# Kernel tuning notes

Hardware: AMD Instinct MI355X
Metric: run time of the kernel (lower is better)

Reference implementation:

```python
import jax, jax.numpy as jnp
import numpy as np

B, L, C = 4, 4096, 1024
H = 16
D = C // H  # head_dim = 64


def setup_inputs() -> dict:
    key = jax.random.key(0)
    k1, k2, k3 = jax.random.split(key, 3)
    x = jax.random.normal(k1, (B, L, C), dtype=jnp.float32)
    W_qkv = jax.random.normal(k2, (C, 3 * C), dtype=jnp.float32) * (C ** -0.5)
    W_proj = jax.random.normal(k3, (C, C), dtype=jnp.float32) * (C ** -0.5)
    b_proj = jnp.zeros((C,), dtype=jnp.float32)
    return {"x": x, "W_qkv": W_qkv, "W_proj": W_proj, "b_proj": b_proj}


def reference(x, W_qkv, W_proj, b_proj):
    Bx, Lx, Cx = x.shape
    # qkv projection (no bias), split into q,k,v each [B, H, L, D]
    qkv = (x @ W_qkv).reshape(Bx, Lx, 3, H, D).transpose(2, 0, 3, 1, 4)
    q, k, v = qkv[0], qkv[1], qkv[2]
    # elu+1 feature map
    q = jax.nn.elu(q) + 1.0
    k = jax.nn.elu(k) + 1.0
    # Faithful to source einsums: kv[b,h,d,m] = sum_n k[b,h,n,d] v[b,h,n,m]
    kv = jnp.einsum('bhnd,bhnm->bhdm', k, v)
    # out[b,h,l,d] = sum_n q[b,h,l,n] * sum_m kv[b,h,d,m] (as written in source)
    out = jnp.einsum('bhln,bhdm->bhld', q, kv)
    out = out.transpose(0, 2, 1, 3).reshape(Bx, Lx, Cx)
    # output projection with bias; dropouts are identity (p=0)
    return out @ W_proj + b_proj
```

## Files before the change

### kernel.cpp

```cpp
#include <hip/hip_runtime.h>
#include <stdint.h>

#define BB 4
#define LL 4096
#define CC 1024
#define HH 16
#define DD 64
#define MTOT (BB*LL)
#define NQK 2048

typedef __attribute__((ext_vector_type(4))) float f32x4;
typedef __attribute__((ext_vector_type(8))) short bf16x8;
typedef __attribute__((ext_vector_type(4))) unsigned short u16x4;
typedef unsigned short u16;

__device__ __forceinline__ u16 f2bf(float f) {
    union { float f; uint32_t u; } v; v.f = f;
    uint32_t r = v.u + 0x7fffu + ((v.u >> 16) & 1u);
    return (u16)(r >> 16);
}
__device__ __forceinline__ float elu1(float s) {
    return s > 0.f ? s + 1.f : __expf(s);
}

__global__ __launch_bounds__(256) void wsum_kernel(const float* __restrict__ Wqkv,
                                                   u16* __restrict__ wvst) {
    int k = blockIdx.x;
    int t = threadIdx.x;
    const f32x4* row = (const f32x4*)(Wqkv + (size_t)k * 3072 + 2048);
    f32x4 v = row[t];
    float s = v.x + v.y + v.z + v.w;
    s += __shfl_xor(s, 1); s += __shfl_xor(s, 2);
    s += __shfl_xor(s, 4); s += __shfl_xor(s, 8);
    if ((t & 15) == 0) {
        int h = t >> 4;
        wvst[h * 1024 + k] = f2bf(s);
    }
}

__global__ void trans_wqk_kernel(const float* __restrict__ Wqkv, u16* __restrict__ wqkt) {
    __shared__ float tile[32][33];
    int n0 = blockIdx.x * 32;
    int k0 = blockIdx.y * 32;
    int tx = threadIdx.x;
    int ty = threadIdx.y;
    #pragma unroll
    for (int i = 0; i < 32; i += 8)
        tile[ty + i][tx] = Wqkv[(size_t)(k0 + ty + i) * 3072 + n0 + tx];
    __syncthreads();
    #pragma unroll
    for (int i = 0; i < 32; i += 8)
        wqkt[(size_t)(n0 + ty + i) * 1024 + k0 + tx] = f2bf(tile[tx][ty + i]);
}

__global__ __launch_bounds__(256) void cast_vsum_kernel(const float* __restrict__ x,
                                                        const u16* __restrict__ wvst,
                                                        u16* __restrict__ xb,
                                                        float* __restrict__ vsum) {
    __shared__ u16 xs[64][136];
    const int t = threadIdx.x;
    const int m0 = blockIdx.x * 64;
    const int w = t >> 6, lane = t & 63;
    const int r = lane & 15, g = lane >> 4;
    f32x4 acc = {0.f, 0.f, 0.f, 0.f};
    for (int k0 = 0; k0 < 1024; k0 += 128) {
        #pragma unroll
        for (int i = 0; i < 8; ++i) {
            const int flat4 = i * 256 + t;
            const int row = flat4 >> 5, c4 = flat4 & 31;
            f32x4 v = *(const f32x4*)(x + (size_t)(m0 + row) * 1024 + k0 + c4 * 4);
            u16x4 o;
            o.x = f2bf(v.x); o.y = f2bf(v.y); o.z = f2bf(v.z); o.w = f2bf(v.w);
            *(u16x4*)(xb + (size_t)(m0 + row) * 1024 + k0 + c4 * 4) = o;
            *(u16x4*)(&xs[row][c4 * 4]) = o;
        }
        __syncthreads();
        #pragma unroll
        for (int ks = 0; ks < 4; ++ks) {
            bf16x8 a = *(const bf16x8*)(&xs[w * 16 + r][ks * 32 + g * 8]);
            bf16x8 b = *(const bf16x8*)(wvst + (size_t)r * 1024 + k0 + ks * 32 + g * 8);
            acc = __builtin_amdgcn_mfma_f32_16x16x32_bf16(a, b, acc, 0, 0, 0);
        }
        __syncthreads();
    }
    #pragma unroll
    for (int ri = 0; ri < 4; ++ri)
        vsum[(size_t)(m0 + w * 16 + g * 4 + ri) * 16 + r] = acc[ri];
}

__global__ __launch_bounds__(512, 4) void gemm_qk_kernel(const u16* __restrict__ A,
                                                         const u16* __restrict__ Bt,
                                                         const float* __restrict__ vsum,
                                                         float* __restrict__ qsum,
                                                         float* __restrict__ kvsum) {
    __shared__ u16 As[2][256 * 32];
    __shared__ u16 Bs[2][128 * 32];
    const int tid = threadIdx.x;
    const int lane = tid & 63;
    const int wid = tid >> 6;
    const int wm = wid >> 1;
    const int wn = wid & 1;
    const int r = lane & 15;
    const int gq = lane >> 4;

    const int wg = blockIdx.x;
    const int swz = (wg & 7) * 128 + (wg >> 3);
    const int bx = swz >> 4;
    const int by = swz & 15;
    const int m0 = bx * 256;
    const int n0 = by * 128;

    const int srow = tid >> 2;
    const int scol = ((tid & 3) ^ (srow & 3)) * 8;
    const u16* aSrc = A + (size_t)(m0 + srow) * 1024 + scol;
    const u16* bSrc = Bt + (size_t)(n0 + srow) * 1024 + scol;
    const int t8 = tid * 8;

#define GL(gp, lp) __builtin_amdgcn_global_load_lds(                                  \
        (const __attribute__((address_space(1))) void*)(gp),                          \
        (__attribute__((address_space(3))) void*)(lp), 16, 0, 0)
#define STAGE(D, KT) do {                                                             \
        GL(aSrc + (KT), &As[D][t8]);                                                  \
        GL(aSrc + 128 * 1024 + (KT), &As[D][t8 + 4096]);                              \
        GL(bSrc + (KT), &Bs[D][t8]);                                                  \
    } while (0)

    f32x4 acc[4][4];
    #pragma unroll
    for (int i = 0; i < 4; ++i)
        #pragma unroll
        for (int j = 0; j < 4; ++j)
            acc[i][j] = (f32x4){0.f, 0.f, 0.f, 0.f};

    const int sk = ((gq) ^ (r & 3)) * 8;

    STAGE(0, 0);
    asm volatile("s_waitcnt vmcnt(0)" ::: "memory");
    __builtin_amdgcn_s_barrier();

    int cur = 0;
    for (int t = 0; t < 32; ++t) {
        if (t + 1 < 32) STAGE(cur ^ 1, (t + 1) * 32);

        bf16x8 a[4], b[4];
        const u16* ap = &As[cur][(wm * 64 + r) * 32];
        const u16* bp = &Bs[cur][(wn * 64 + r) * 32];
        #pragma unroll
        for (int mi = 0; mi < 4; ++mi) a[mi] = *(const bf16x8*)(ap + mi * 512 + sk);
        #pragma unroll
        for (int ni = 0; ni < 4; ++ni) b[ni] = *(const bf16x8*)(bp + ni * 512 + sk);

        __builtin_amdgcn_s_setprio(1);
        #pragma unroll
        for (int mi = 0; mi < 4; ++mi)
            #pragma unroll
            for (int ni = 0; ni < 4; ++ni)
                acc[mi][ni] = __builtin_amdgcn_mfma_f32_16x16x32_bf16(a[mi], b[ni], acc[mi][ni], 0, 0, 0);
        __builtin_amdgcn_s_setprio(0);

        asm volatile("s_waitcnt vmcnt(0)" ::: "memory");
        __builtin_amdgcn_s_barrier();
        cur ^= 1;
    }
#undef STAGE
#undef GL

    if (by < 8) {
        const int h = by * 2 + wn;
        #pragma unroll
        for (int mi = 0; mi < 4; ++mi)
            #pragma unroll
            for (int rr = 0; rr < 4; ++rr) {
                float s = elu1(acc[mi][0][rr]) + elu1(acc[mi][1][rr]) +
                          elu1(acc[mi][2][rr]) + elu1(acc[mi][3][rr]);
                s += __shfl_xor(s, 1); s += __shfl_xor(s, 2);
                s += __shfl_xor(s, 4); s += __shfl_xor(s, 8);
                if (r == 0)
                    qsum[(size_t)(m0 + wm * 64 + mi * 16 + gq * 4 + rr) * 16 + h] = s;
            }
    } else {
        const int h = (by - 8) * 2 + wn;
        const int b = m0 >> 12;
        float kvp[4] = {0.f, 0.f, 0.f, 0.f};
        #pragma unroll
        for (int mi = 0; mi < 4; ++mi)
            #pragma unroll
            for (int rr = 0; rr < 4; ++rr) {
                const int row = m0 + wm * 64 + mi * 16 + gq * 4 + rr;
                const float vs = vsum[(size_t)row * 16 + h];
                #pragma unroll
                for (int nj = 0; nj < 4; ++nj)
                    kvp[nj] += elu1(acc[mi][nj][rr]) * vs;
            }
        #pragma unroll
        for (int nj = 0; nj < 4; ++nj) {
            kvp[nj] += __shfl_xor(kvp[nj], 16);
            kvp[nj] += __shfl_xor(kvp[nj], 32);
        }
        if (gq == 0) {
            #pragma unroll
            for (int nj = 0; nj < 4; ++nj)
                atomicAdd(&kvsum[((size_t)b * 16 + h) * 64 + nj * 16 + r], kvp[nj]);
        }
    }
}

__global__ __launch_bounds__(256) void wkv_kernel(const float* __restrict__ kvsum,
                                                  const float* __restrict__ Wproj,
                                                  float* __restrict__ wkv) {
    __shared__ float kv[64];
    const int bh = blockIdx.y;
    const int c = blockIdx.x * 256 + threadIdx.x;
    if (threadIdx.x < 64) kv[threadIdx.x] = kvsum[bh * 64 + threadIdx.x];
    __syncthreads();
    const int h = bh & 15;
    float s = 0.f;
    #pragma unroll 8
    for (int d = 0; d < 64; ++d)
        s += kv[d] * Wproj[(size_t)(h * 64 + d) * 1024 + c];
    wkv[(size_t)bh * 1024 + c] = s;
}

__global__ __launch_bounds__(256) void final_kernel(const float* __restrict__ qsum,
                                                    const float* __restrict__ wkv,
                                                    const float* __restrict__ bproj,
                                                    float* __restrict__ y) {
    __shared__ float qs[4][16];
    const int r0 = blockIdx.x * 4;
    const int t = threadIdx.x;
    if (t < 64) qs[t >> 4][t & 15] = qsum[(size_t)(r0 + (t >> 4)) * 16 + (t & 15)];
    __syncthreads();
    const int b = r0 >> 12;
    const f32x4* wk4 = (const f32x4*)(wkv + (size_t)b * 16 * 1024);
    f32x4 bp = ((const f32x4*)bproj)[t];
    f32x4 a0 = bp, a1 = bp, a2 = bp, a3 = bp;
    #pragma unroll
    for (int h = 0; h < 16; ++h) {
        f32x4 w = wk4[h * 256 + t];
        a0 += qs[0][h] * w;
        a1 += qs[1][h] * w;
        a2 += qs[2][h] * w;
        a3 += qs[3][h] * w;
    }
    f32x4* y4 = (f32x4*)y;
    y4[(size_t)(r0 + 0) * 256 + t] = a0;
    y4[(size_t)(r0 + 1) * 256 + t] = a1;
    y4[(size_t)(r0 + 2) * 256 + t] = a2;
    y4[(size_t)(r0 + 3) * 256 + t] = a3;
}

extern "C" void kernel_launch(void* const* d_in, const int* in_sizes, int n_in,
                              void* d_out, int out_size, void* d_ws, size_t ws_size,
                              hipStream_t stream) {
    const float* x     = (const float*)d_in[0];
    const float* Wqkv  = (const float*)d_in[1];
    const float* Wproj = (const float*)d_in[2];
    const float* bproj = (const float*)d_in[3];
    float* y = (float*)d_out;

    char* ws = (char*)d_ws;
    u16*   xb    = (u16*)(ws);
    u16*   wqkt  = (u16*)(ws + 33554432);
    u16*   wvst  = (u16*)(ws + 37748736);
    float* vsum  = (float*)(ws + 37781504);
    float* qsum  = (float*)(ws + 38830080);
    float* kvsum = (float*)(ws + 39878656);
    float* wkv   = (float*)(ws + 39895040);

    hipMemsetAsync(kvsum, 0, 4096 * sizeof(float), stream);

    wsum_kernel<<<1024, 256, 0, stream>>>(Wqkv, wvst);
    trans_wqk_kernel<<<dim3(64, 32), dim3(32, 8), 0, stream>>>(Wqkv, wqkt);
    cast_vsum_kernel<<<256, 256, 0, stream>>>(x, wvst, xb, vsum);
    gemm_qk_kernel<<<1024, 512, 0, stream>>>(xb, wqkt, vsum, qsum, kvsum);
    wkv_kernel<<<dim3(4, 64), 256, 0, stream>>>(kvsum, Wproj, wkv);
    final_kernel<<<4096, 256, 0, stream>>>(qsum, wkv, bproj, y);
}
```

Measured before the change: 154.2 us.

## Shrink QK GEMM tile to 128x128 with 256 threads and unroll double buffer

The QK GEMM block tile drops from 256x128 with 8 waves to 128x128 with 4 waves, and the grid doubles to 2048 blocks with an adjusted swizzle. The LDS XOR swizzle now uses bits 2-3 of the row instead of bits 0-1, and the k-loop is unrolled by two so the buffer index is a compile-time constant. The aim is more resident blocks per CU and fewer LDS bank conflicts. In exchange, each block reuses its loaded data less, so global and L2 traffic per FLOP goes up.

```diff
diff --git a/kernel.cpp b/kernel.cpp
--- a/kernel.cpp
+++ b/kernel.cpp
@@ -88,30 +88,30 @@
         vsum[(size_t)(m0 + w * 16 + g * 4 + ri) * 16 + r] = acc[ri];
 }
 
-__global__ __launch_bounds__(512, 4) void gemm_qk_kernel(const u16* __restrict__ A,
+__global__ __launch_bounds__(256, 4) void gemm_qk_kernel(const u16* __restrict__ A,
                                                          const u16* __restrict__ Bt,
                                                          const float* __restrict__ vsum,
                                                          float* __restrict__ qsum,
                                                          float* __restrict__ kvsum) {
-    __shared__ u16 As[2][256 * 32];
+    __shared__ u16 As[2][128 * 32];
     __shared__ u16 Bs[2][128 * 32];
     const int tid = threadIdx.x;
     const int lane = tid & 63;
-    const int wid = tid >> 6;
-    const int wm = wid >> 1;
-    const int wn = wid & 1;
+    const int w = tid >> 6;
+    const int wm = w >> 1;
+    const int wn = w & 1;
     const int r = lane & 15;
     const int gq = lane >> 4;
 
     const int wg = blockIdx.x;
-    const int swz = (wg & 7) * 128 + (wg >> 3);
-    const int bx = swz >> 4;
-    const int by = swz & 15;
-    const int m0 = bx * 256;
+    const int s = (wg & 7) * 256 + (wg >> 3);
+    const int bx = s >> 4;
+    const int by = s & 15;
+    const int m0 = bx * 128;
     const int n0 = by * 128;
 
     const int srow = tid >> 2;
-    const int scol = ((tid & 3) ^ (srow & 3)) * 8;
+    const int scol = ((tid & 3) ^ ((srow >> 2) & 3)) * 8;
     const u16* aSrc = A + (size_t)(m0 + srow) * 1024 + scol;
     const u16* bSrc = Bt + (size_t)(n0 + srow) * 1024 + scol;
     const int t8 = tid * 8;
@@ -121,8 +121,9 @@
         (__attribute__((address_space(3))) void*)(lp), 16, 0, 0)
 #define STAGE(D, KT) do {                                                             \
         GL(aSrc + (KT), &As[D][t8]);                                                  \
-        GL(aSrc + 128 * 1024 + (KT), &As[D][t8 + 4096]);                              \
+        GL(aSrc + 64 * 1024 + (KT), &As[D][t8 + 2048]);                               \
         GL(bSrc + (KT), &Bs[D][t8]);                                                  \
+        GL(bSrc + 64 * 1024 + (KT), &Bs[D][t8 + 2048]);                               \
     } while (0)
 
     f32x4 acc[4][4];
@@ -132,36 +133,38 @@
         for (int j = 0; j < 4; ++j)
             acc[i][j] = (f32x4){0.f, 0.f, 0.f, 0.f};
 
-    const int sk = ((gq) ^ (r & 3)) * 8;
+    const int sk = (gq ^ ((r >> 2) & 3)) * 8;
 
     STAGE(0, 0);
     asm volatile("s_waitcnt vmcnt(0)" ::: "memory");
     __builtin_amdgcn_s_barrier();
 
-    int cur = 0;
-    for (int t = 0; t < 32; ++t) {
-        if (t + 1 < 32) STAGE(cur ^ 1, (t + 1) * 32);
-
-        bf16x8 a[4], b[4];
-        const u16* ap = &As[cur][(wm * 64 + r) * 32];
-        const u16* bp = &Bs[cur][(wn * 64 + r) * 32];
-        #pragma unroll
-        for (int mi = 0; mi < 4; ++mi) a[mi] = *(const bf16x8*)(ap + mi * 512 + sk);
-        #pragma unroll
-        for (int ni = 0; ni < 4; ++ni) b[ni] = *(const bf16x8*)(bp + ni * 512 + sk);
-
-        __builtin_amdgcn_s_setprio(1);
-        #pragma unroll
-        for (int mi = 0; mi < 4; ++mi)
-            #pragma unroll
-            for (int ni = 0; ni < 4; ++ni)
-                acc[mi][ni] = __builtin_amdgcn_mfma_f32_16x16x32_bf16(a[mi], b[ni], acc[mi][ni], 0, 0, 0);
-        __builtin_amdgcn_s_setprio(0);
-
-        asm volatile("s_waitcnt vmcnt(0)" ::: "memory");
-        __builtin_amdgcn_s_barrier();
-        cur ^= 1;
-    }
+#define BODY(T, CUR) do {                                                             \
+        if ((T) + 1 < 32) STAGE((CUR) ^ 1, ((T) + 1) * 32);                           \
+        bf16x8 a[4], b[4];                                                            \
+        const u16* ap = &As[CUR][(wm * 64 + r) * 32 + sk];                            \
+        const u16* bp = &Bs[CUR][(wn * 64 + r) * 32 + sk];                            \
+        _Pragma("unroll")                                                             \
+        for (int mi = 0; mi < 4; ++mi) a[mi] = *(const bf16x8*)(ap + mi * 512);       \
+        _Pragma("unroll")                                                             \
+        for (int ni = 0; ni < 4; ++ni) b[ni] = *(const bf16x8*)(bp + ni * 512);       \
+        __builtin_amdgcn_s_setprio(1);                                                \
+        _Pragma("unroll")                                                             \
+        for (int mi = 0; mi < 4; ++mi)                                                \
+            _Pragma("unroll")                                                         \
+            for (int ni = 0; ni < 4; ++ni)                                            \
+                acc[mi][ni] = __builtin_amdgcn_mfma_f32_16x16x32_bf16(                \
+                    a[mi], b[ni], acc[mi][ni], 0, 0, 0);                              \
+        __builtin_amdgcn_s_setprio(0);                                                \
+        asm volatile("s_waitcnt vmcnt(0)" ::: "memory");                              \
+        __builtin_amdgcn_s_barrier();                                                 \
+    } while (0)
+
+    for (int t = 0; t < 32; t += 2) {
+        BODY(t, 0);
+        BODY(t + 1, 1);
+    }
+#undef BODY
 #undef STAGE
 #undef GL
 
@@ -171,12 +174,12 @@
         for (int mi = 0; mi < 4; ++mi)
             #pragma unroll
             for (int rr = 0; rr < 4; ++rr) {
-                float s = elu1(acc[mi][0][rr]) + elu1(acc[mi][1][rr]) +
-                          elu1(acc[mi][2][rr]) + elu1(acc[mi][3][rr]);
-                s += __shfl_xor(s, 1); s += __shfl_xor(s, 2);
-                s += __shfl_xor(s, 4); s += __shfl_xor(s, 8);
+                float sv = elu1(acc[mi][0][rr]) + elu1(acc[mi][1][rr]) +
+                           elu1(acc[mi][2][rr]) + elu1(acc[mi][3][rr]);
+                sv += __shfl_xor(sv, 1); sv += __shfl_xor(sv, 2);
+                sv += __shfl_xor(sv, 4); sv += __shfl_xor(sv, 8);
                 if (r == 0)
-                    qsum[(size_t)(m0 + wm * 64 + mi * 16 + gq * 4 + rr) * 16 + h] = s;
+                    qsum[(size_t)(m0 + wm * 64 + mi * 16 + gq * 4 + rr) * 16 + h] = sv;
             }
     } else {
         const int h = (by - 8) * 2 + wn;
@@ -272,7 +275,7 @@
     wsum_kernel<<<1024, 256, 0, stream>>>(Wqkv, wvst);
     trans_wqk_kernel<<<dim3(64, 32), dim3(32, 8), 0, stream>>>(Wqkv, wqkt);
     cast_vsum_kernel<<<256, 256, 0, stream>>>(x, wvst, xb, vsum);
-    gemm_qk_kernel<<<1024, 512, 0, stream>>>(xb, wqkt, vsum, qsum, kvsum);
+    gemm_qk_kernel<<<2048, 256, 0, stream>>>(xb, wqkt, vsum, qsum, kvsum);
     wkv_kernel<<<dim3(4, 64), 256, 0, stream>>>(kvsum, Wproj, wkv);
     final_kernel<<<4096, 256, 0, stream>>>(qsum, wkv, bproj, y);
 }
```

New measurement: 159.6 us. 1.03x slower.
